# Performance work log

Measured on AMD Instinct MI355X. Metric: run time of the kernel, lower is better.

The kernel has to match this reference:

```python
import jax, jax.numpy as jnp
import numpy as np

UNITS = 128
FILTERS = 32
KSIZE = 31
B, T, DV, DQ = 64, 1000, 512, 1024


def setup_inputs() -> dict:
    key = jax.random.key(0)
    ks = jax.random.split(key, 12)
    scale = 0.05
    inp = {
        "query": jax.random.normal(ks[0], (B, DQ), jnp.float32),
        "values": jax.random.normal(ks[1], (B, T, DV), jnp.float32),
        "previous_attention_weights": jax.random.uniform(ks[2], (B, T, 1), jnp.float32),
        # learned params
        "Wq": jax.random.normal(ks[3], (DQ, UNITS), jnp.float32) * scale,
        "bq": jnp.zeros((UNITS,), jnp.float32),
        "Wm": jax.random.normal(ks[4], (DV, UNITS), jnp.float32) * scale,
        "bm": jnp.zeros((UNITS,), jnp.float32),
        "Wv": jax.random.normal(ks[5], (UNITS, 1), jnp.float32) * scale,
        "bv": jnp.zeros((1,), jnp.float32),
        "Wconv": jax.random.normal(ks[6], (KSIZE, 1, FILTERS), jnp.float32) * scale,  # [W, Cin, Cout]
        "Wl": jax.random.normal(ks[7], (FILTERS, UNITS), jnp.float32) * scale,
    }
    return inp


def _forward(query, values, prev_w, Wq, bq, Wm, bm, Wv, bv, Wconv, Wl):
    # location features: Conv1D (same padding, no bias) then Dense(tanh, no bias)
    loc = jax.lax.conv_general_dilated(
        prev_w, Wconv, window_strides=(1,), padding="SAME",
        dimension_numbers=("NWC", "WIO", "NWC"))          # [B, T, FILTERS]
    loc = jnp.tanh(loc @ Wl)                                # [B, T, UNITS]
    q = query @ Wq + bq                                     # [B, UNITS]
    m = values @ Wm + bm                                    # [B, T, UNITS]
    score = jnp.tanh(m + q[:, None, :] + loc) @ Wv + bv     # [B, T, 1]
    attention_weights = jax.nn.softmax(score, axis=1)       # softmax over time
    context = jnp.sum(attention_weights * values, axis=1)   # [B, DV]
    return context, attention_weights


def reference(query, values, previous_attention_weights, Wq, bq, Wm, bm, Wv, bv, Wconv, Wl):
    return _forward(query, values, previous_attention_weights,
                    Wq, bq, Wm, bm, Wv, bv, Wconv, Wl)
```

## Files before the change

kernel.cpp:

```cpp
#include <hip/hip_runtime.h>

#define B_  64
#define T_  1000
#define DV_ 512
#define DQ_ 1024
#define U_  128
#define F_  32
#define KS_ 31
#define P_  16
#define CT_ 63

typedef __attribute__((ext_vector_type(8))) short short8;
typedef __attribute__((ext_vector_type(4))) float f32x4;

__device__ __forceinline__ unsigned pk2(float a, float b) {
    union { float f; unsigned u; } x, y;
    x.f = a; y.f = b;
    unsigned ra = (x.u + 0x7FFFu + ((x.u >> 16) & 1u)) >> 16;
    unsigned rb = (y.u + 0x7FFFu + ((y.u >> 16) & 1u)) >> 16;
    return (ra & 0xFFFFu) | (rb << 16);
}

__device__ __forceinline__ float fast_tanh(float x) {
    return 1.0f - 2.0f / (__expf(2.0f * x) + 1.0f);
}

__device__ __forceinline__ short8 pk8(float4 f0, float4 f1) {
    int4 q;
    q.x = pk2(f0.x, f0.y); q.y = pk2(f0.z, f0.w);
    q.z = pk2(f1.x, f1.y); q.w = pk2(f1.z, f1.w);
    return *(short8*)&q;
}

__global__ __launch_bounds__(1024) void prep_kernel(
    const float* __restrict__ Wm, const float* __restrict__ Wl,
    const float* __restrict__ query, const float* __restrict__ Wq,
    short* __restrict__ WmX, short* __restrict__ WlX, float* __restrict__ partQ)
{
    __shared__ float sh[1024];
    int blk = blockIdx.x, tid = threadIdx.x;
    if (blk < 9) {
        int g = blk * 1024 + tid;
        if (g < 8192) {
            int kc = g >> 9, e = g & 511;
            int n = e >> 2, q = e & 3;
            int kb = kc * 32 + q * 8;
            int4 p;
            p.x = pk2(Wm[(kb + 0) * U_ + n], Wm[(kb + 1) * U_ + n]);
            p.y = pk2(Wm[(kb + 2) * U_ + n], Wm[(kb + 3) * U_ + n]);
            p.z = pk2(Wm[(kb + 4) * U_ + n], Wm[(kb + 5) * U_ + n]);
            p.w = pk2(Wm[(kb + 6) * U_ + n], Wm[(kb + 7) * U_ + n]);
            ((int4*)WmX)[g] = p;
        } else if (g < 8704) {
            int e = g - 8192;
            int n = e >> 2, q = e & 3;
            int kb = q * 8;
            int4 p;
            p.x = pk2(Wl[(kb + 0) * U_ + n], Wl[(kb + 1) * U_ + n]);
            p.y = pk2(Wl[(kb + 2) * U_ + n], Wl[(kb + 3) * U_ + n]);
            p.z = pk2(Wl[(kb + 4) * U_ + n], Wl[(kb + 5) * U_ + n]);
            p.w = pk2(Wl[(kb + 6) * U_ + n], Wl[(kb + 7) * U_ + n]);
            ((int4*)WlX)[e] = p;
        }
    } else {
        int id = blk - 9;
        int s  = id >> 2;
        int bg = id & 3;
        sh[tid] = query[(size_t)(bg * 16 + (tid >> 6)) * DQ_ + s * 64 + (tid & 63)];
        __syncthreads();
        int u = tid & 127, h = tid >> 7;
        const float* wp = Wq + (size_t)(s * 64) * U_ + u;
        const float* q0 = sh + (h * 2) * 64;
        const float* q1 = q0 + 64;
        float a0 = 0.f, a1 = 0.f;
#pragma unroll 8
        for (int k = 0; k < 64; ++k) {
            float w = wp[(size_t)k * U_];
            a0 += q0[k] * w; a1 += q1[k] * w;
        }
        int b0i = bg * 16 + h * 2;
        partQ[s * 8192 + b0i * 128 + u]       = a0;
        partQ[s * 8192 + (b0i + 1) * 128 + u] = a1;
    }
}

__global__ __launch_bounds__(256) void score_kernel(
    const float* __restrict__ values, const float* __restrict__ prev,
    const float* __restrict__ Wc, const float* __restrict__ Wv,
    const float* __restrict__ bv, const short* __restrict__ WmX,
    const short* __restrict__ WlX, const float* __restrict__ partQ,
    const float* __restrict__ bq, const float* __restrict__ bm,
    float* __restrict__ scores)
{
    __shared__ float WcS[KS_ * F_];
    __shared__ short AsL[64 * 32];
    __shared__ float qbS[2 * U_];
    __shared__ float WvS[U_];

    const int tid = threadIdx.x;
    const int r0 = blockIdx.x * 64;
    const int b0 = r0 / T_;
    const int b1 = (r0 + 63) / T_;

    for (int i = tid; i < KS_ * F_; i += 256) WcS[i] = Wc[i];
    if (tid < U_) WvS[tid] = Wv[tid];
    {
        int u = tid & (U_ - 1);
        int bb = (tid < U_) ? b0 : b1;
        float s = bq[u] + bm[u];
#pragma unroll
        for (int sl = 0; sl < 16; ++sl) s += partQ[sl * 8192 + bb * 128 + u];
        qbS[tid] = s;
    }

    const int wv = tid >> 6, lane = tid & 63;
    const int quad = lane >> 4, m15 = lane & 15;
    const int row0 = wv * 16 + m15;
    const float* aP = values + (size_t)(r0 + row0) * DV_ + quad * 8;
    const int4* bW  = (const int4*)WmX + m15 * 4 + quad;
    const int4* blW = (const int4*)WlX + m15 * 4 + quad;

    float4 aq0[2], aq1[2], aq2[2], aqn[2];
    int4 bf[2][8];
    aq0[0] = *(const float4*)(aP);      aq0[1] = *(const float4*)(aP + 4);
    aq1[0] = *(const float4*)(aP + 32); aq1[1] = *(const float4*)(aP + 36);
    aq2[0] = *(const float4*)(aP + 64); aq2[1] = *(const float4*)(aP + 68);
#pragma unroll
    for (int c = 0; c < 8; ++c) bf[0][c] = bW[c * 64];
#pragma unroll
    for (int c = 0; c < 8; ++c) bf[1][c] = bW[512 + c * 64];

    __syncthreads();

    {
        int i = tid & 63, fg = tid >> 6;
        int r = r0 + i;
        int b = r / T_;
        int t = r - b * T_;
        const float* pv = prev + b * T_;
        float a8[8] = {};
#pragma unroll
        for (int k = 0; k < KS_; ++k) {
            int tt = t + k - 15;
            float p = ((unsigned)tt < (unsigned)T_) ? pv[tt] : 0.f;
#pragma unroll
            for (int j = 0; j < 8; ++j) a8[j] += p * WcS[k * F_ + fg * 8 + j];
        }
        int4 pq;
        pq.x = pk2(a8[0], a8[1]); pq.y = pk2(a8[2], a8[3]);
        pq.z = pk2(a8[4], a8[5]); pq.w = pk2(a8[6], a8[7]);
        ((int4*)AsL)[i * 4 + (fg ^ ((i >> 1) & 3))] = pq;
    }
    __syncthreads();

    f32x4 acc[8] = {};
    {
        short8 afl = ((const short8*)AsL)[row0 * 4 + (quad ^ ((row0 >> 1) & 3))];
#pragma unroll
        for (int c = 0; c < 8; ++c) {
            int4 bl = blW[c * 64];
            acc[c] = __builtin_amdgcn_mfma_f32_16x16x32_bf16(afl, *(short8*)&bl, acc[c], 0, 0, 0);
        }
        int qoff[4];
#pragma unroll
        for (int v = 0; v < 4; ++v) {
            int r = r0 + wv * 16 + quad * 4 + v;
            qoff[v] = ((r / T_) == b0) ? 0 : U_;
        }
#pragma unroll
        for (int c = 0; c < 8; ++c) {
            int col = c * 16 + m15;
#pragma unroll
            for (int v = 0; v < 4; ++v)
                acc[c][v] = qbS[qoff[v] + col] + fast_tanh(acc[c][v]);
        }
    }

#pragma unroll
    for (int kc = 0; kc < 16; ++kc) {
        if (kc + 3 < 16) {
            aqn[0] = *(const float4*)(aP + (kc + 3) * 32);
            aqn[1] = *(const float4*)(aP + (kc + 3) * 32 + 4);
        }
        short8 af = pk8(aq0[0], aq0[1]);
#pragma unroll
        for (int c = 0; c < 8; ++c) {
            acc[c] = __builtin_amdgcn_mfma_f32_16x16x32_bf16(af, *(short8*)&bf[kc & 1][c], acc[c], 0, 0, 0);
            if (kc + 2 < 16) bf[kc & 1][c] = bW[(kc + 2) * 512 + c * 64];
        }
        aq0[0] = aq1[0]; aq0[1] = aq1[1];
        aq1[0] = aq2[0]; aq1[1] = aq2[1];
        aq2[0] = aqn[0]; aq2[1] = aqn[1];
    }

    float psum[4] = {};
#pragma unroll
    for (int c = 0; c < 8; ++c) {
        int col = c * 16 + m15;
        float wvv = WvS[col];
#pragma unroll
        for (int v = 0; v < 4; ++v)
            psum[v] += fast_tanh(acc[c][v]) * wvv;
    }
#pragma unroll
    for (int off = 1; off < 16; off <<= 1) {
#pragma unroll
        for (int v = 0; v < 4; ++v) psum[v] += __shfl_xor(psum[v], off);
    }
    if (m15 == 0) {
        float bvv = bv[0];
#pragma unroll
        for (int v = 0; v < 4; ++v)
            scores[r0 + wv * 16 + quad * 4 + v] = psum[v] + bvv;
    }
}

__global__ __launch_bounds__(256) void ctx_kernel(
    const float* __restrict__ values, const float* __restrict__ scores,
    float* __restrict__ attw, float* __restrict__ ctx)
{
    __shared__ float wS[CT_];
    __shared__ float4 ps[128];
    __shared__ float red[4];
    int b = blockIdx.x, p = blockIdx.y, tid = threadIdx.x;
    const float* sb = scores + b * T_;

    float v[4];
    int tv[4];
#pragma unroll
    for (int i = 0; i < 4; ++i) {
        int t = tid + i * 256;
        tv[i] = t;
        v[i] = (t < T_) ? sb[t] : -1e30f;
    }
    float mx = fmaxf(fmaxf(v[0], v[1]), fmaxf(v[2], v[3]));
#pragma unroll
    for (int off = 32; off >= 1; off >>= 1) mx = fmaxf(mx, __shfl_xor(mx, off));
    int wvi = tid >> 6, lane = tid & 63;
    if (lane == 0) red[wvi] = mx;
    __syncthreads();
    mx = fmaxf(fmaxf(red[0], red[1]), fmaxf(red[2], red[3]));
    float sum = 0.f;
#pragma unroll
    for (int i = 0; i < 4; ++i)
        sum += (tv[i] < T_) ? __expf(v[i] - mx) : 0.f;
#pragma unroll
    for (int off = 32; off >= 1; off >>= 1) sum += __shfl_xor(sum, off);
    __syncthreads();
    if (lane == 0) red[wvi] = sum;
    __syncthreads();
    float inv = 1.0f / (red[0] + red[1] + red[2] + red[3]);

    int t0 = p * CT_;
    int len = (T_ - t0 < CT_) ? (T_ - t0) : CT_;
    if (tid < len) {
        float e = __expf(sb[t0 + tid] - mx) * inv;
        wS[tid] = e;
        attw[b * T_ + t0 + tid] = e;
    }
    __syncthreads();

    int cl = tid & 127, tp = tid >> 7;
    const float* vp = values + ((size_t)b * T_ + t0) * DV_ + cl * 4;
    float4 a = {0.f, 0.f, 0.f, 0.f};
#pragma unroll 4
    for (int t = tp; t < len; t += 2) {
        float4 vv = *(const float4*)(vp + (size_t)t * DV_);
        float wt = wS[t];
        a.x += wt * vv.x; a.y += wt * vv.y; a.z += wt * vv.z; a.w += wt * vv.w;
    }
    if (tp == 1) ps[cl] = a;
    __syncthreads();
    if (tp == 0) {
        float4 o = ps[cl];
        o.x += a.x; o.y += a.y; o.z += a.z; o.w += a.w;
        float* cp = ctx + (size_t)b * DV_ + cl * 4;
        atomicAdd(cp + 0, o.x);
        atomicAdd(cp + 1, o.y);
        atomicAdd(cp + 2, o.z);
        atomicAdd(cp + 3, o.w);
    }
}

extern "C" void kernel_launch(void* const* d_in, const int* in_sizes, int n_in,
                              void* d_out, int out_size, void* d_ws, size_t ws_size,
                              hipStream_t stream) {
    const float* query  = (const float*)d_in[0];
    const float* values = (const float*)d_in[1];
    const float* prev   = (const float*)d_in[2];
    const float* Wq     = (const float*)d_in[3];
    const float* bq     = (const float*)d_in[4];
    const float* Wm     = (const float*)d_in[5];
    const float* bm     = (const float*)d_in[6];
    const float* Wv     = (const float*)d_in[7];
    const float* bv     = (const float*)d_in[8];
    const float* Wc     = (const float*)d_in[9];
    const float* Wl     = (const float*)d_in[10];

    float* out  = (float*)d_out;
    float* ctx  = out;
    float* attw = out + B_ * DV_;

    char* ws = (char*)d_ws;
    float* partQ  = (float*)(ws);
    float* scores = (float*)(ws + 2097152);
    short* WmX    = (short*)(ws + 2097152 + 262144);
    short* WlX    = (short*)(ws + 2097152 + 262144 + 131072);

    hipMemsetAsync(ctx, 0, B_ * DV_ * sizeof(float), stream);
    prep_kernel<<<73, 1024, 0, stream>>>(Wm, Wl, query, Wq, WmX, WlX, partQ);
    score_kernel<<<1000, 256, 0, stream>>>(values, prev, Wc, Wv, bv, WmX, WlX,
                                           partQ, bq, bm, scores);
    ctx_kernel<<<dim3(B_, P_), 256, 0, stream>>>(values, scores, attw, ctx);
}
```

Baseline: 273.1 us.

## Stage Wm weight tiles in LDS via async global_load_lds double buffering

The bf16-packed Wm operand is no longer loaded by every wave directly from global memory into registers. The block now copies it cooperatively into a 32 KB double-buffered LDS area with global_load_lds, prefetching the next slice while the current one feeds the MFMAs. An XOR swizzle is applied when Wm is packed in the prep kernel so the LDS reads avoid bank conflicts. This removes the redundant per-wave global/L2 traffic and frees registers, at the cost of more LDS per block (possibly lower occupancy) and extra barriers per stage.

```diff
diff --git a/kernel.cpp b/kernel.cpp
--- a/kernel.cpp
+++ b/kernel.cpp
@@ -50,7 +50,7 @@
             p.y = pk2(Wm[(kb + 2) * U_ + n], Wm[(kb + 3) * U_ + n]);
             p.z = pk2(Wm[(kb + 4) * U_ + n], Wm[(kb + 5) * U_ + n]);
             p.w = pk2(Wm[(kb + 6) * U_ + n], Wm[(kb + 7) * U_ + n]);
-            ((int4*)WmX)[g] = p;
+            ((int4*)WmX)[g ^ ((g >> 3) & 7)] = p;
         } else if (g < 8704) {
             int e = g - 8192;
             int n = e >> 2, q = e & 3;
@@ -96,11 +96,31 @@
     __shared__ short AsL[64 * 32];
     __shared__ float qbS[2 * U_];
     __shared__ float WvS[U_];
+    __shared__ __align__(16) short Bs[2 * 8192];
 
     const int tid = threadIdx.x;
     const int r0 = blockIdx.x * 64;
     const int b0 = r0 / T_;
     const int b1 = (r0 + 63) / T_;
+
+    const int wv = tid >> 6, lane = tid & 63;
+    const int quad = lane >> 4, m15 = lane & 15;
+
+    const char* WmB = (const char*)WmX;
+    char* BsC = (char*)Bs;
+
+#pragma unroll
+    for (int r = 0; r < 4; ++r) {
+        const char* s0 = WmB + r * 4096 + wv * 1024 + lane * 16;
+        char* d0 = BsC + r * 4096 + wv * 1024;
+        __builtin_amdgcn_global_load_lds((const unsigned*)s0, (unsigned*)d0, 16, 0, 0);
+    }
+#pragma unroll
+    for (int r = 0; r < 4; ++r) {
+        const char* s1 = WmB + 16384 + r * 4096 + wv * 1024 + lane * 16;
+        char* d1 = BsC + 16384 + r * 4096 + wv * 1024;
+        __builtin_amdgcn_global_load_lds((const unsigned*)s1, (unsigned*)d1, 16, 0, 0);
+    }
 
     for (int i = tid; i < KS_ * F_; i += 256) WcS[i] = Wc[i];
     if (tid < U_) WvS[tid] = Wv[tid];
@@ -113,22 +133,14 @@
         qbS[tid] = s;
     }
 
-    const int wv = tid >> 6, lane = tid & 63;
-    const int quad = lane >> 4, m15 = lane & 15;
     const int row0 = wv * 16 + m15;
     const float* aP = values + (size_t)(r0 + row0) * DV_ + quad * 8;
-    const int4* bW  = (const int4*)WmX + m15 * 4 + quad;
     const int4* blW = (const int4*)WlX + m15 * 4 + quad;
-
-    float4 aq0[2], aq1[2], aq2[2], aqn[2];
-    int4 bf[2][8];
+    const int sgg = (m15 * 4 + quad) ^ (m15 >> 1);
+
+    float4 aq0[2], aq1[2], aq2[2];
     aq0[0] = *(const float4*)(aP);      aq0[1] = *(const float4*)(aP + 4);
     aq1[0] = *(const float4*)(aP + 32); aq1[1] = *(const float4*)(aP + 36);
-    aq2[0] = *(const float4*)(aP + 64); aq2[1] = *(const float4*)(aP + 68);
-#pragma unroll
-    for (int c = 0; c < 8; ++c) bf[0][c] = bW[c * 64];
-#pragma unroll
-    for (int c = 0; c < 8; ++c) bf[1][c] = bW[512 + c * 64];
 
     __syncthreads();
 
@@ -177,20 +189,33 @@
     }
 
 #pragma unroll
-    for (int kc = 0; kc < 16; ++kc) {
-        if (kc + 3 < 16) {
-            aqn[0] = *(const float4*)(aP + (kc + 3) * 32);
-            aqn[1] = *(const float4*)(aP + (kc + 3) * 32 + 4);
-        }
-        short8 af = pk8(aq0[0], aq0[1]);
-#pragma unroll
-        for (int c = 0; c < 8; ++c) {
-            acc[c] = __builtin_amdgcn_mfma_f32_16x16x32_bf16(af, *(short8*)&bf[kc & 1][c], acc[c], 0, 0, 0);
-            if (kc + 2 < 16) bf[kc & 1][c] = bW[(kc + 2) * 512 + c * 64];
-        }
-        aq0[0] = aq1[0]; aq0[1] = aq1[1];
-        aq1[0] = aq2[0]; aq1[1] = aq2[1];
-        aq2[0] = aqn[0]; aq2[1] = aqn[1];
+    for (int p = 0; p < 8; ++p) {
+        if (p >= 1 && p + 1 < 8) {
+#pragma unroll
+            for (int r = 0; r < 4; ++r) {
+                const char* s = WmB + (p + 1) * 16384 + r * 4096 + wv * 1024 + lane * 16;
+                char* d = BsC + ((p + 1) & 1) * 16384 + r * 4096 + wv * 1024;
+                __builtin_amdgcn_global_load_lds((const unsigned*)s, (unsigned*)d, 16, 0, 0);
+            }
+        }
+        const short8* bb = (const short8*)(BsC + (p & 1) * 16384);
+#pragma unroll
+        for (int i = 0; i < 2; ++i) {
+            const int kc = p * 2 + i;
+            if (kc + 2 < 16) {
+                aq2[0] = *(const float4*)(aP + (kc + 2) * 32);
+                aq2[1] = *(const float4*)(aP + (kc + 2) * 32 + 4);
+            }
+            short8 af = pk8(aq0[0], aq0[1]);
+#pragma unroll
+            for (int c = 0; c < 8; ++c) {
+                short8 bfc = bb[i * 512 + c * 64 + sgg];
+                acc[c] = __builtin_amdgcn_mfma_f32_16x16x32_bf16(af, bfc, acc[c], 0, 0, 0);
+            }
+            aq0[0] = aq1[0]; aq0[1] = aq1[1];
+            aq1[0] = aq2[0]; aq1[1] = aq2[1];
+        }
+        if (p < 7) __syncthreads();
     }
 
     float psum[4] = {};
```

New measurement: 277.1 us. No clear change (+1.4%).

## Split score kernel work across column halves with smaller row tiles

Applied to the files above, without the earlier changes.

Halves the row tile per block from 64 to 32 and assigns pairs of waves to the same 16 rows, each computing half of the 128 output units, with partial scores combined through shared memory. The grid doubles to 2000 blocks, and per-thread register use falls (4 accumulators and a single-buffered B fragment) to allow more parallelism and occupancy. In exchange, each values row is read twice (once per column-half wave), prefetch depth is reduced, and an extra barrier plus reduction is added.

```diff
diff --git a/kernel.cpp b/kernel.cpp
--- a/kernel.cpp
+++ b/kernel.cpp
@@ -93,14 +93,15 @@
     float* __restrict__ scores)
 {
     __shared__ float WcS[KS_ * F_];
-    __shared__ short AsL[64 * 32];
+    __shared__ short AsL[32 * 32];
     __shared__ float qbS[2 * U_];
     __shared__ float WvS[U_];
+    __shared__ float sred[2][2][16];
 
     const int tid = threadIdx.x;
-    const int r0 = blockIdx.x * 64;
+    const int r0 = blockIdx.x * 32;
     const int b0 = r0 / T_;
-    const int b1 = (r0 + 63) / T_;
+    const int b1 = (r0 + 31) / T_;
 
     for (int i = tid; i < KS_ * F_; i += 256) WcS[i] = Wc[i];
     if (tid < U_) WvS[tid] = Wv[tid];
@@ -115,25 +116,23 @@
 
     const int wv = tid >> 6, lane = tid & 63;
     const int quad = lane >> 4, m15 = lane & 15;
-    const int row0 = wv * 16 + m15;
+    const int rg = wv >> 1, cg = wv & 1;
+    const int row0 = rg * 16 + m15;
     const float* aP = values + (size_t)(r0 + row0) * DV_ + quad * 8;
-    const int4* bW  = (const int4*)WmX + m15 * 4 + quad;
-    const int4* blW = (const int4*)WlX + m15 * 4 + quad;
-
-    float4 aq0[2], aq1[2], aq2[2], aqn[2];
-    int4 bf[2][8];
+    const int4* bW  = (const int4*)WmX + cg * 256 + m15 * 4 + quad;
+    const int4* blW = (const int4*)WlX + cg * 256 + m15 * 4 + quad;
+
+    float4 aq0[2], aq1[2], aq2[2];
+    int4 bf[4];
     aq0[0] = *(const float4*)(aP);      aq0[1] = *(const float4*)(aP + 4);
     aq1[0] = *(const float4*)(aP + 32); aq1[1] = *(const float4*)(aP + 36);
-    aq2[0] = *(const float4*)(aP + 64); aq2[1] = *(const float4*)(aP + 68);
-#pragma unroll
-    for (int c = 0; c < 8; ++c) bf[0][c] = bW[c * 64];
-#pragma unroll
-    for (int c = 0; c < 8; ++c) bf[1][c] = bW[512 + c * 64];
-
-    __syncthreads();
-
-    {
-        int i = tid & 63, fg = tid >> 6;
+#pragma unroll
+    for (int c = 0; c < 4; ++c) bf[c] = bW[c * 64];
+
+    __syncthreads();
+
+    if (tid < 128) {
+        int i = tid & 31, fg = tid >> 5;
         int r = r0 + i;
         int b = r / T_;
         int t = r - b * T_;
@@ -153,23 +152,23 @@
     }
     __syncthreads();
 
-    f32x4 acc[8] = {};
+    f32x4 acc[4] = {};
     {
         short8 afl = ((const short8*)AsL)[row0 * 4 + (quad ^ ((row0 >> 1) & 3))];
 #pragma unroll
-        for (int c = 0; c < 8; ++c) {
+        for (int c = 0; c < 4; ++c) {
             int4 bl = blW[c * 64];
             acc[c] = __builtin_amdgcn_mfma_f32_16x16x32_bf16(afl, *(short8*)&bl, acc[c], 0, 0, 0);
         }
         int qoff[4];
 #pragma unroll
         for (int v = 0; v < 4; ++v) {
-            int r = r0 + wv * 16 + quad * 4 + v;
+            int r = r0 + rg * 16 + quad * 4 + v;
             qoff[v] = ((r / T_) == b0) ? 0 : U_;
         }
 #pragma unroll
-        for (int c = 0; c < 8; ++c) {
-            int col = c * 16 + m15;
+        for (int c = 0; c < 4; ++c) {
+            int col = (cg * 4 + c) * 16 + m15;
 #pragma unroll
             for (int v = 0; v < 4; ++v)
                 acc[c][v] = qbS[qoff[v] + col] + fast_tanh(acc[c][v]);
@@ -178,25 +177,24 @@
 
 #pragma unroll
     for (int kc = 0; kc < 16; ++kc) {
-        if (kc + 3 < 16) {
-            aqn[0] = *(const float4*)(aP + (kc + 3) * 32);
-            aqn[1] = *(const float4*)(aP + (kc + 3) * 32 + 4);
+        if (kc + 2 < 16) {
+            aq2[0] = *(const float4*)(aP + (kc + 2) * 32);
+            aq2[1] = *(const float4*)(aP + (kc + 2) * 32 + 4);
         }
         short8 af = pk8(aq0[0], aq0[1]);
 #pragma unroll
-        for (int c = 0; c < 8; ++c) {
-            acc[c] = __builtin_amdgcn_mfma_f32_16x16x32_bf16(af, *(short8*)&bf[kc & 1][c], acc[c], 0, 0, 0);
-            if (kc + 2 < 16) bf[kc & 1][c] = bW[(kc + 2) * 512 + c * 64];
+        for (int c = 0; c < 4; ++c) {
+            acc[c] = __builtin_amdgcn_mfma_f32_16x16x32_bf16(af, *(short8*)&bf[c], acc[c], 0, 0, 0);
+            if (kc + 1 < 16) bf[c] = bW[(kc + 1) * 512 + c * 64];
         }
         aq0[0] = aq1[0]; aq0[1] = aq1[1];
         aq1[0] = aq2[0]; aq1[1] = aq2[1];
-        aq2[0] = aqn[0]; aq2[1] = aqn[1];
     }
 
     float psum[4] = {};
 #pragma unroll
-    for (int c = 0; c < 8; ++c) {
-        int col = c * 16 + m15;
+    for (int c = 0; c < 4; ++c) {
+        int col = (cg * 4 + c) * 16 + m15;
         float wvv = WvS[col];
 #pragma unroll
         for (int v = 0; v < 4; ++v)
@@ -208,10 +206,13 @@
         for (int v = 0; v < 4; ++v) psum[v] += __shfl_xor(psum[v], off);
     }
     if (m15 == 0) {
-        float bvv = bv[0];
-#pragma unroll
-        for (int v = 0; v < 4; ++v)
-            scores[r0 + wv * 16 + quad * 4 + v] = psum[v] + bvv;
+#pragma unroll
+        for (int v = 0; v < 4; ++v) sred[rg][cg][quad * 4 + v] = psum[v];
+    }
+    __syncthreads();
+    if (tid < 32) {
+        int rgg = tid >> 4, r = tid & 15;
+        scores[r0 + rgg * 16 + r] = sred[rgg][0][r] + sred[rgg][1][r] + bv[0];
     }
 }
 
@@ -309,7 +310,7 @@
 
     hipMemsetAsync(ctx, 0, B_ * DV_ * sizeof(float), stream);
     prep_kernel<<<73, 1024, 0, stream>>>(Wm, Wl, query, Wq, WmX, WlX, partQ);
-    score_kernel<<<1000, 256, 0, stream>>>(values, prev, Wc, Wv, bv, WmX, WlX,
+    score_kernel<<<2000, 256, 0, stream>>>(values, prev, Wc, Wv, bv, WmX, WlX,
                                            partQ, bq, bm, scores);
     ctx_kernel<<<dim3(B_, P_), 256, 0, stream>>>(values, scores, attw, ctx);
 }
```

After: 320.4 us. 1.17x slower.
